# Kernel tuning notes

Hardware: AMD Instinct MI355X
Metric: run time of the kernel (lower is better)

Reference implementation:

```python
import jax, jax.numpy as jnp
import numpy as np

AVGF = 30   # number of averaged temporal segments (timesteps of the TTM)
TK = 10     # hardcoded number of transformer 'layers' in the source
HA = 1      # hardcoded number of heads


def _ln(v, g, b, eps=1e-5):
    # LayerNorm over the last (only) dim of a 1-D vector
    mu = jnp.mean(v)
    var = jnp.mean((v - mu) ** 2)
    return (v - mu) / jnp.sqrt(var + eps) * g + b


def setup_inputs() -> dict:
    key = jax.random.key(0)
    ks = jax.random.split(key, 8)
    C, S, T = 32, 32, 360
    M = C * S  # 1024 = M_size1
    sc = 0.02  # scale randn params for numerical sanity (source uses raw randn)
    x = jax.random.normal(ks[0], (C, S, T), jnp.float32)
    weight = jax.random.normal(ks[1], (M, M), jnp.float32) * sc
    Wq = jax.random.normal(ks[2], (TK, HA, M // HA, M), jnp.float32) * sc
    Wk = jax.random.normal(ks[3], (TK, HA, M // HA, M), jnp.float32) * sc
    Wv = jax.random.normal(ks[4], (TK, HA, M // HA, M), jnp.float32) * sc
    Wo = jax.random.normal(ks[5], (TK, M, M), jnp.float32) * sc
    ln_g = jnp.ones((M,), jnp.float32); ln_b = jnp.zeros((M,), jnp.float32)
    lnz_g = jnp.ones((M,), jnp.float32); lnz_b = jnp.zeros((M,), jnp.float32)
    fc1_w = jax.random.normal(ks[6], (4 * M, M), jnp.float32) * sc
    fc1_b = jnp.zeros((4 * M,), jnp.float32)
    fc2_w = jax.random.normal(ks[7], (M, 4 * M), jnp.float32) * sc
    fc2_b = jnp.zeros((M,), jnp.float32)
    return dict(x=x, weight=weight, Wq=Wq, Wk=Wk, Wv=Wv, Wo=Wo,
                ln_g=ln_g, ln_b=ln_b, lnz_g=lnz_g, lnz_b=lnz_b,
                fc1_w=fc1_w, fc1_b=fc1_b, fc2_w=fc2_w, fc2_b=fc2_b)


def reference(x, weight, Wq, Wk, Wv, Wo, ln_g, ln_b, lnz_g, lnz_b,
              fc1_w, fc1_b, fc2_w, fc2_b):
    C, S, T = x.shape
    M = C * S
    seg = T // AVGF
    Dh = M // HA
    # redefine(): transpose(0,2) then segment-average over the temporal dim, flatten
    xcf = jnp.transpose(x, (2, 1, 0)).reshape(AVGF, seg, S * C).mean(axis=1)  # (AVGF, M)
    # sinusoidal positional 'bias' exactly as the source loop builds it
    i = jnp.arange(AVGF, dtype=jnp.float32)[:, None]
    j = jnp.arange(0, M, 2, dtype=jnp.float32)[None, :]
    ang = i / jnp.power(jnp.float32(10000.0), 2.0 * j / M)
    pe = jnp.zeros((AVGF, M), jnp.float32).at[:, 0::2].set(jnp.sin(ang)).at[:, 1::2].set(jnp.cos(ang))
    s0 = xcf @ weight.T + pe  # savespace init: weight @ x[i] + bias
    scale = 1.0 / jnp.sqrt(jnp.float32(Dh))

    def step(vcum, s):
        # vcum[a]: sum over previously processed timesteps of r*v at layer a
        for a in range(TK):
            z = _ln(s, ln_g, ln_b)
            q = jnp.einsum('hdm,m->hd', Wq[a], z)  # (HA, Dh)
            k = jnp.einsum('hdm,m->hd', Wk[a], z)
            v = jnp.einsum('hdm,m->hd', Wv[a], z)
            score = jnp.sum(q * scale * k, axis=-1)          # (HA,) scalar per head
            r = jax.nn.softmax(score[:, None], axis=-1)[:, 0]  # softmax of a scalar == 1
            rv = r[:, None] * v
            s = Wo[a] @ vcum[a].reshape(-1) + s              # imv = sum over subj < i
            s = _ln(s, lnz_g, lnz_b) + s
            s = fc2_w @ jax.nn.gelu(fc1_w @ s + fc1_b, approximate=False) + fc2_b
            vcum = vcum.at[a].add(rv)                        # current timestep now visible to future
        return vcum, s

    vcum0 = jnp.zeros((TK, HA, Dh), jnp.float32)
    _, out = jax.lax.scan(step, vcum0, s0)  # sequential over timesteps
    return out.reshape(AVGF, S, C)
```

## Files before the change

### kernel.cpp

```cpp
#include <hip/hip_runtime.h>

#define MDIM 1024
#define H4   4096
#define TKL  10
#define NT   30
#define NWFR 39
#define GBLK 256
#define GTHR 1024
#define AGENT __HIP_MEMORY_SCOPE_AGENT

typedef _Float16 h2v __attribute__((ext_vector_type(2)));
typedef unsigned int uv4 __attribute__((ext_vector_type(4)));
typedef float fv4 __attribute__((ext_vector_type(4)));
union U16 { uv4 u; h2v h[4]; _Float16 f[8]; };

__device__ __forceinline__ float wred(float v) {
#pragma unroll
  for (int o = 32; o; o >>= 1) v += __shfl_xor(v, o, 64);
  return v;
}

__device__ __forceinline__ float dot16(const U16& w, const U16& x, float acc) {
  acc = __builtin_amdgcn_fdot2(w.h[0], x.h[0], acc, false);
  acc = __builtin_amdgcn_fdot2(w.h[1], x.h[1], acc, false);
  acc = __builtin_amdgcn_fdot2(w.h[2], x.h[2], acc, false);
  acc = __builtin_amdgcn_fdot2(w.h[3], x.h[3], acc, false);
  return acc;
}

__device__ __forceinline__ void stg16(const void* p, uv4 v) {
  asm volatile("global_store_dwordx4 %0, %1, off sc0 sc1" :: "v"(p), "v"(v) : "memory");
}

__global__ void k_cvt(const float* __restrict__ in, _Float16* __restrict__ out, int n8) {
  int g = blockIdx.x * blockDim.x + threadIdx.x;
  if (g >= n8) return;
  const float4* p = (const float4*)in;
  float4 a = p[2 * g], b = p[2 * g + 1];
  U16 o;
  o.f[0] = (_Float16)a.x; o.f[1] = (_Float16)a.y;
  o.f[2] = (_Float16)a.z; o.f[3] = (_Float16)a.w;
  o.f[4] = (_Float16)b.x; o.f[5] = (_Float16)b.y;
  o.f[6] = (_Float16)b.z; o.f[7] = (_Float16)b.w;
  ((uv4*)out)[g] = o.u;
}

__global__ void k_xcf(const float* __restrict__ x, float* __restrict__ xcf) {
  int idx = blockIdx.x * blockDim.x + threadIdx.x;
  if (idx >= NT * MDIM) return;
  int i = idx >> 10, m = idx & (MDIM - 1);
  int c = m & 31, s = m >> 5;
  const float* p = x + c * (32 * 360) + s * 360 + i * 12;
  float acc = 0.f;
#pragma unroll
  for (int k = 0; k < 12; ++k) acc += p[k];
  xcf[idx] = acc * (1.0f / 12.0f);
}

__global__ void k_s0(const float* __restrict__ xcf, const float* __restrict__ W,
                     float* __restrict__ S, float* __restrict__ Smir) {
  int wid = (blockIdx.x * blockDim.x + threadIdx.x) >> 6;
  int lane = threadIdx.x & 63;
  if (wid >= NT * MDIM) return;
  int i = wid >> 10, m = wid & (MDIM - 1);
  const float4* wr = (const float4*)(W + (size_t)m * MDIM);
  const float4* xr = (const float4*)(xcf + i * MDIM);
  float acc = 0.f;
#pragma unroll
  for (int k = 0; k < 4; ++k) {
    float4 w = wr[lane + (k << 6)];
    float4 xv = xr[lane + (k << 6)];
    acc += w.x * xv.x + w.y * xv.y + w.z * xv.z + w.w * xv.w;
  }
  acc = wred(acc);
  if (lane == 0) {
    int e = m & ~1;
    float ang = (float)i / powf(10000.0f, (float)e / 512.0f);
    float pe = (m & 1) ? cosf(ang) : sinf(ang);
    float val = acc + pe;
    S[wid] = val;
    Smir[((size_t)i * NT + i) * MDIM + m] = val;
  }
}

__device__ __forceinline__ void gbar(unsigned* bar, unsigned ep) {
  asm volatile("s_waitcnt vmcnt(0)" ::: "memory");
  __syncthreads();
  if (threadIdx.x == 0) {
    unsigned* leaf = bar + ((blockIdx.x & 7) << 5);
    const unsigned prev = __hip_atomic_fetch_add(leaf, 1u, __ATOMIC_RELAXED, AGENT);
    if (prev == ep * 32u - 1u) {
      const unsigned r = __hip_atomic_fetch_add(bar + 256, 1u, __ATOMIC_RELAXED, AGENT);
      if (r == ep * 8u - 1u)
        __hip_atomic_store(bar + 288, ep, __ATOMIC_RELAXED, AGENT);
    }
    while (__hip_atomic_load(bar + 288, __ATOMIC_RELAXED, AGENT) < ep)
      __builtin_amdgcn_s_sleep(2);
  }
  __syncthreads();
}

__global__ __launch_bounds__(GTHR) void k_main(
    const _Float16* __restrict__ Wvh, const _Float16* __restrict__ Woh,
    const _Float16* __restrict__ fc1h, const float* __restrict__ fc1b,
    const _Float16* __restrict__ fc2h, const float* __restrict__ fc2b,
    const float* __restrict__ lng, const float* __restrict__ lnb,
    const float* __restrict__ lzg, const float* __restrict__ lzb,
    float* __restrict__ S, float* __restrict__ ocum,
    float* __restrict__ Smir, float* __restrict__ Omir, float* __restrict__ vmir,
    _Float16* __restrict__ hmir, unsigned* __restrict__ bar) {
  __shared__ __align__(16) _Float16 WoL[32 * MDIM];
  __shared__ __align__(16) _Float16 fc1L[16 * MDIM];
  __shared__ __align__(16) _Float16 fc2L[4 * H4];
  __shared__ __align__(16) _Float16 zxL[10 * MDIM];
  __shared__ __align__(16) float4 stats[TKL];
  __shared__ __align__(16) float vOut[40];
  __shared__ __align__(16) _Float16 hgel[TKL][16];
  __shared__ float part[4][4][TKL];
  __shared__ __align__(16) float sOut[TKL][4];
  _Float16* zL = zxL;
  _Float16* x2L = zxL + 5 * MDIM;
  _Float16* vL = zxL;

  const int tid = threadIdx.x;
  const int lane = tid & 63;
  const int bwave = tid >> 6;
  const int b = blockIdx.x;
  unsigned ep = 0;

  __builtin_amdgcn_fence(__ATOMIC_ACQUIRE, "agent");

#pragma unroll
  for (int it = 0; it < 2; ++it) {
    const int idx = tid + (it << 10);
    ((uv4*)fc1L)[idx] = ((const uv4*)(fc1h + (size_t)b * 16384))[idx];
    ((uv4*)fc2L)[idx] = ((const uv4*)(fc2h + (size_t)b * 16384))[idx];
  }
#pragma unroll
  for (int it = 0; it < 4; ++it) {
    const int idx = tid + (it << 10);
    const int row = idx >> 7, off = idx & 127;
    const int layer = row >> 2, q = row & 3;
    ((uv4*)WoL)[idx] =
        *(const uv4*)(Woh + ((size_t)layer << 20) + ((size_t)((b << 2) + q) << 10) + (off << 3));
  }
  __syncthreads();

  for (int t = 0; t < NWFR; ++t) {
    const int alo = (t - (NT - 1)) > 0 ? (t - (NT - 1)) : 0;
    const int ahi = t < (TKL - 1) ? t : (TKL - 1);
    const int nc = ahi - alo + 1;
    const float* Smirt = Smir + (size_t)t * NT * MDIM;
    const float* Omirt = Omir + (size_t)t * TKL * MDIM;

    if (bwave < nc) {
      const int a = alo + bwave, i = t - a;
      const fv4* sp = (const fv4*)(Smirt + (size_t)i * MDIM + (lane << 4));
      const fv4* op = (const fv4*)(Omirt + (size_t)a * MDIM + (lane << 4));
      fv4 sv[4], tv[4];
#pragma unroll
      for (int k = 0; k < 4; ++k) { sv[k] = sp[k]; tv[k] = sv[k] + op[k]; }
      float s1 = 0.f, t1 = 0.f;
#pragma unroll
      for (int k = 0; k < 4; ++k)
#pragma unroll
        for (int e = 0; e < 4; ++e) { s1 += sv[k][e]; t1 += tv[k][e]; }
      const float mu_s = wred(s1) * (1.0f / MDIM);
      const float mu_t = wred(t1) * (1.0f / MDIM);
      float s2 = 0.f, t2 = 0.f;
#pragma unroll
      for (int k = 0; k < 4; ++k)
#pragma unroll
        for (int e = 0; e < 4; ++e) {
          float d = sv[k][e] - mu_s; s2 += d * d;
          float f = tv[k][e] - mu_t; t2 += f * f;
        }
      const float var_s = wred(s2) * (1.0f / MDIM);
      const float var_t = wred(t2) * (1.0f / MDIM);
      if (!lane)
        stats[bwave] = make_float4(mu_s, rsqrtf(var_s + 1e-5f),
                                   mu_t, rsqrtf(var_t + 1e-5f));
    }
    __syncthreads();

#pragma unroll
    for (int ch = 0; ch < 2; ++ch) {
      const int c0 = ch * 5;
      if (c0 < nc) {
        {
          const int cp = tid >> 7, e = (tid & 127) << 3;
          const int c = c0 + cp;
          if (cp < 5 && c < nc) {
            const int a = alo + c, i = t - a;
            const float4 st4 = stats[c];
            fv4 sA = *(const fv4*)(Smirt + (size_t)i * MDIM + e);
            fv4 sB = *(const fv4*)(Smirt + (size_t)i * MDIM + e + 4);
            fv4 oA = *(const fv4*)(Omirt + (size_t)a * MDIM + e);
            fv4 oB = *(const fv4*)(Omirt + (size_t)a * MDIM + e + 4);
            fv4 g1A = *(const fv4*)(lng + e), g1B = *(const fv4*)(lng + e + 4);
            fv4 b1A = *(const fv4*)(lnb + e), b1B = *(const fv4*)(lnb + e + 4);
            fv4 g2A = *(const fv4*)(lzg + e), g2B = *(const fv4*)(lzg + e + 4);
            fv4 b2A = *(const fv4*)(lzb + e), b2B = *(const fv4*)(lzb + e + 4);
            U16 zz, xx;
#pragma unroll
            for (int k = 0; k < 4; ++k) {
              zz.f[k] = (_Float16)((sA[k] - st4.x) * st4.y * g1A[k] + b1A[k]);
              zz.f[4 + k] = (_Float16)((sB[k] - st4.x) * st4.y * g1B[k] + b1B[k]);
              const float u0 = sA[k] + oA[k], u1 = sB[k] + oB[k];
              xx.f[k] = (_Float16)((u0 - st4.z) * st4.w * g2A[k] + b2A[k] + u0);
              xx.f[4 + k] = (_Float16)((u1 - st4.z) * st4.w * g2B[k] + b2B[k] + u1);
            }
            *(uv4*)(zL + cp * MDIM + e) = zz.u;
            *(uv4*)(x2L + cp * MDIM + e) = xx.u;
          }
        }
        __syncthreads();
        {
          const int rw = bwave;
          U16 f0, f1;
          f0.u = *(const uv4*)(fc1L + rw * MDIM + (lane << 3));
          f1.u = *(const uv4*)(fc1L + rw * MDIM + 512 + (lane << 3));
          float sel = 0.f;
#pragma unroll
          for (int cc = 0; cc < 5; ++cc) {
            const int c = c0 + cc;
            if (c < nc) {
              U16 x0, x1;
              x0.u = *(const uv4*)(x2L + cc * MDIM + (lane << 3));
              x1.u = *(const uv4*)(x2L + cc * MDIM + 512 + (lane << 3));
              float acc = dot16(f0, x0, 0.f);
              acc = dot16(f1, x1, acc);
              acc = wred(acc);
              sel = (lane == cc) ? acc : sel;
            }
          }
          const float xg = sel + fc1b[(b << 4) | rw];
          const float ge = 0.5f * xg * (1.0f + erff(xg * 0.70710678118654752f));
          if (lane < 5 && c0 + lane < nc) hgel[c0 + lane][rw] = (_Float16)ge;
        }
#pragma unroll
        for (int k = 0; k < 2; ++k) {
          const int j = bwave + (k << 4);
          if (j < 20) {
            const int rc = j >> 2, c = c0 + rc;
            if (c < nc) {
              const int layer = alo + c;
              if (t - layer != NT - 1) {
                const _Float16* wp = Wvh + ((size_t)layer << 20) +
                                     ((size_t)((b << 2) + (j & 3)) << 10);
                U16 w0, w1, z0, z1;
                w0.u = *(const uv4*)(wp + (lane << 3));
                w1.u = *(const uv4*)(wp + 512 + (lane << 3));
                z0.u = *(const uv4*)(zL + rc * MDIM + (lane << 3));
                z1.u = *(const uv4*)(zL + rc * MDIM + 512 + (lane << 3));
                float acc = dot16(w0, z0, 0.f);
                acc = dot16(w1, z1, acc);
                acc = wred(acc);
                if (!lane) vOut[(c << 2) + (j & 3)] = acc;
              }
            }
          }
        }
        __syncthreads();
      }
    }
    if (tid < TKL && tid < nc && (t - (alo + tid)) != NT - 1)
      stg16(vmir + ((size_t)t * TKL + alo + tid) * MDIM + (b << 2),
            __builtin_bit_cast(uv4, *(const fv4*)&vOut[tid << 2]));
    if (bwave < nc && lane < 2)
      stg16(hmir + ((size_t)t * TKL + alo + bwave) * H4 + (b << 4) + (lane << 3),
            *(const uv4*)&hgel[bwave][lane << 3]);
    ++ep; gbar(bar, ep);

#pragma unroll
    for (int c = 0; c < TKL; ++c)
      if (c < nc && (t - (alo + c)) != NT - 1)
        vL[c * MDIM + tid] = (_Float16)vmir[((size_t)t * TKL + alo + c) * MDIM + tid];
    __syncthreads();
#pragma unroll
    for (int k = 0; k < 3; ++k) {
      const int j = bwave + (k << 4);
      if (j < 40) {
        const int c = j >> 2;
        if (c < nc) {
          const int layer = alo + c;
          if (layer < 8 && t - layer != NT - 1) {
            const _Float16* wp = WoL + ((layer << 2) + (j & 3)) * MDIM;
            U16 w0, w1, v0, v1;
            w0.u = *(const uv4*)(wp + (lane << 3));
            w1.u = *(const uv4*)(wp + 512 + (lane << 3));
            v0.u = *(const uv4*)(vL + c * MDIM + (lane << 3));
            v1.u = *(const uv4*)(vL + c * MDIM + 512 + (lane << 3));
            float acc = dot16(w0, v0, 0.f);
            acc = dot16(w1, v1, acc);
            acc = wred(acc);
            if (!lane) vOut[j] = acc;
          }
        }
      }
    }
#pragma unroll
    for (int k = 0; k < 3; ++k) {
      const int j = bwave + (k << 4);
      if (j < 40) {
        const int c = j >> 2;
        if (c < nc) {
          const int layer = alo + c;
          if (layer >= 8 && t - layer != NT - 1) {
            const _Float16* wp = Woh + ((size_t)layer << 20) +
                                 ((size_t)((b << 2) + (j & 3)) << 10);
            U16 w0, w1, v0, v1;
            w0.u = *(const uv4*)(wp + (lane << 3));
            w1.u = *(const uv4*)(wp + 512 + (lane << 3));
            v0.u = *(const uv4*)(vL + c * MDIM + (lane << 3));
            v1.u = *(const uv4*)(vL + c * MDIM + 512 + (lane << 3));
            float acc = dot16(w0, v0, 0.f);
            acc = dot16(w1, v1, acc);
            acc = wred(acc);
            if (!lane) vOut[j] = acc;
          }
        }
      }
    }
    {
      const int rl = bwave >> 2, kq = bwave & 3;
      U16 w2a, w2b;
      w2a.u = *(const uv4*)(fc2L + rl * H4 + (kq << 10) + (lane << 3));
      w2b.u = *(const uv4*)(fc2L + rl * H4 + (kq << 10) + 512 + (lane << 3));
#pragma unroll
      for (int c = 0; c < TKL; ++c)
        if (c < nc) {
          U16 h0, h1;
          const _Float16* hp = hmir + ((size_t)t * TKL + alo + c) * H4 + (kq << 10);
          h0.u = *(const uv4*)(hp + (lane << 3));
          h1.u = *(const uv4*)(hp + 512 + (lane << 3));
          float acc = dot16(w2a, h0, 0.f);
          acc = dot16(w2b, h1, acc);
          acc = wred(acc);
          if (!lane) part[rl][kq][c] = acc;
        }
    }
    __syncthreads();
    if (tid < TKL && tid < nc && (t - (alo + tid)) != NT - 1) {
      const int layer = alo + tid;
      float* po = ocum + layer * MDIM + (b << 2);
      fv4 o = *(const fv4*)po;
      o += *(const fv4*)&vOut[tid << 2];
      *(fv4*)po = o;
      stg16(Omir + ((size_t)(t + 1) * TKL + layer) * MDIM + (b << 2),
            __builtin_bit_cast(uv4, o));
    }
    if (bwave < nc && lane < 4)
      sOut[bwave][lane] = part[lane][0][bwave] + part[lane][1][bwave] +
                          part[lane][2][bwave] + part[lane][3][bwave] +
                          fc2b[(b << 2) | lane];
    __syncthreads();
    if (bwave < nc && !lane) {
      const int a = alo + bwave, i = t - a;
      fv4 sv = *(const fv4*)(&sOut[bwave][0]);
      if (a == TKL - 1)
        *(fv4*)(S + (size_t)i * MDIM + (b << 2)) = sv;
      else
        stg16(Smir + ((size_t)(t + 1) * NT + i) * MDIM + (b << 2),
              __builtin_bit_cast(uv4, sv));
    }
    ++ep; gbar(bar, ep);
  }
}

extern "C" void kernel_launch(void* const* d_in, const int* in_sizes, int n_in,
                              void* d_out, int out_size, void* d_ws, size_t ws_size,
                              hipStream_t stream) {
  const float* x    = (const float*)d_in[0];
  const float* W    = (const float*)d_in[1];
  const float* Wv   = (const float*)d_in[4];
  const float* Wo   = (const float*)d_in[5];
  const float* lng  = (const float*)d_in[6];
  const float* lnb  = (const float*)d_in[7];
  const float* lzg  = (const float*)d_in[8];
  const float* lzb  = (const float*)d_in[9];
  const float* fc1w = (const float*)d_in[10];
  const float* fc1b = (const float*)d_in[11];
  const float* fc2w = (const float*)d_in[12];
  const float* fc2b = (const float*)d_in[13];
  float* S = (float*)d_out;

  float* xcf  = (float*)d_ws;
  float* ocum = xcf + 30720;
  unsigned* bar = (unsigned*)(ocum + 10240);
  float* Smir = (float*)(bar + 512);
  float* Omir = Smir + 1228800;
  float* vmir = Omir + 409600;
  _Float16* hmir = (_Float16*)(vmir + 409600);
  _Float16* Wvh  = hmir + 1638400;
  _Float16* Woh  = Wvh + 10485760;
  _Float16* fc1h = Woh + 10485760;
  _Float16* fc2h = fc1h + 4194304;

  hipLaunchKernelGGL(k_cvt, dim3(5120), dim3(256), 0, stream, Wv, Wvh, 1310720);
  hipLaunchKernelGGL(k_cvt, dim3(5120), dim3(256), 0, stream, Wo, Woh, 1310720);
  hipLaunchKernelGGL(k_cvt, dim3(2048), dim3(256), 0, stream, fc1w, fc1h, 524288);
  hipLaunchKernelGGL(k_cvt, dim3(2048), dim3(256), 0, stream, fc2w, fc2h, 524288);
  hipLaunchKernelGGL(k_xcf, dim3((NT * MDIM + 255) / 256), dim3(256), 0, stream, x, xcf);
  hipLaunchKernelGGL(k_s0, dim3(NT * MDIM / 4), dim3(256), 0, stream, xcf, W, S, Smir);
  hipMemsetAsync(ocum, 0, 10240 * sizeof(float), stream);
  hipMemsetAsync(Omir, 0, 409600 * sizeof(float), stream);
  hipMemsetAsync(bar, 0, 2048, stream);

  hipLaunchKernelGGL(k_main, dim3(GBLK), dim3(GTHR), 0, stream,
                     Wvh, Woh, fc1h, fc1b, fc2h, fc2b, lng, lnb, lzg, lzb,
                     S, ocum, Smir, Omir, vmir, hmir, bar);
}
```

Before: 862.1 us.

## Use MFMA on a dedicated wave for fc1/fc2 and overlap with Wv/Wo dots

The fc1 and fc2 matrix-vector products, previously spread across all 16 waves with fdot2 and cross-lane reductions, are moved onto wave 0 using 16x16x32 f16 MFMA instructions. The other 15 waves concurrently compute the Wv and Wo dot products. The two 5-column chunks are merged into a single pass with full 10-column LDS buffers, which removes a barrier and the partial-sum reduction stage. fc2 weights are now read from global memory instead of LDS, freeing shared memory. The risk is that one wave serially handles the whole K=4096 fc2 loop and becomes the critical path.

```diff
diff --git a/kernel.cpp b/kernel.cpp
--- a/kernel.cpp
+++ b/kernel.cpp
@@ -10,6 +10,8 @@
 #define AGENT __HIP_MEMORY_SCOPE_AGENT
 
 typedef _Float16 h2v __attribute__((ext_vector_type(2)));
+typedef _Float16 f16x8 __attribute__((ext_vector_type(8)));
+typedef float f32x4 __attribute__((ext_vector_type(4)));
 typedef unsigned int uv4 __attribute__((ext_vector_type(4)));
 typedef float fv4 __attribute__((ext_vector_type(4)));
 union U16 { uv4 u; h2v h[4]; _Float16 f[8]; };
@@ -100,7 +102,7 @@
   __syncthreads();
 }
 
-__global__ __launch_bounds__(GTHR) void k_main(
+__global__ __launch_bounds__(GTHR, 4) void k_main(
     const _Float16* __restrict__ Wvh, const _Float16* __restrict__ Woh,
     const _Float16* __restrict__ fc1h, const float* __restrict__ fc1b,
     const _Float16* __restrict__ fc2h, const float* __restrict__ fc2b,
@@ -111,16 +113,12 @@
     _Float16* __restrict__ hmir, unsigned* __restrict__ bar) {
   __shared__ __align__(16) _Float16 WoL[32 * MDIM];
   __shared__ __align__(16) _Float16 fc1L[16 * MDIM];
-  __shared__ __align__(16) _Float16 fc2L[4 * H4];
-  __shared__ __align__(16) _Float16 zxL[10 * MDIM];
+  __shared__ __align__(16) _Float16 zL[TKL * MDIM];
+  __shared__ __align__(16) _Float16 x2L[TKL * MDIM];
   __shared__ __align__(16) float4 stats[TKL];
   __shared__ __align__(16) float vOut[40];
   __shared__ __align__(16) _Float16 hgel[TKL][16];
-  __shared__ float part[4][4][TKL];
-  __shared__ __align__(16) float sOut[TKL][4];
-  _Float16* zL = zxL;
-  _Float16* x2L = zxL + 5 * MDIM;
-  _Float16* vL = zxL;
+  _Float16* vL = zL;
 
   const int tid = threadIdx.x;
   const int lane = tid & 63;
@@ -134,7 +132,6 @@
   for (int it = 0; it < 2; ++it) {
     const int idx = tid + (it << 10);
     ((uv4*)fc1L)[idx] = ((const uv4*)(fc1h + (size_t)b * 16384))[idx];
-    ((uv4*)fc2L)[idx] = ((const uv4*)(fc2h + (size_t)b * 16384))[idx];
   }
 #pragma unroll
   for (int it = 0; it < 4; ++it) {
@@ -184,86 +181,86 @@
     __syncthreads();
 
 #pragma unroll
-    for (int ch = 0; ch < 2; ++ch) {
-      const int c0 = ch * 5;
-      if (c0 < nc) {
-        {
-          const int cp = tid >> 7, e = (tid & 127) << 3;
-          const int c = c0 + cp;
-          if (cp < 5 && c < nc) {
-            const int a = alo + c, i = t - a;
-            const float4 st4 = stats[c];
-            fv4 sA = *(const fv4*)(Smirt + (size_t)i * MDIM + e);
-            fv4 sB = *(const fv4*)(Smirt + (size_t)i * MDIM + e + 4);
-            fv4 oA = *(const fv4*)(Omirt + (size_t)a * MDIM + e);
-            fv4 oB = *(const fv4*)(Omirt + (size_t)a * MDIM + e + 4);
-            fv4 g1A = *(const fv4*)(lng + e), g1B = *(const fv4*)(lng + e + 4);
-            fv4 b1A = *(const fv4*)(lnb + e), b1B = *(const fv4*)(lnb + e + 4);
-            fv4 g2A = *(const fv4*)(lzg + e), g2B = *(const fv4*)(lzg + e + 4);
-            fv4 b2A = *(const fv4*)(lzb + e), b2B = *(const fv4*)(lzb + e + 4);
-            U16 zz, xx;
-#pragma unroll
-            for (int k = 0; k < 4; ++k) {
-              zz.f[k] = (_Float16)((sA[k] - st4.x) * st4.y * g1A[k] + b1A[k]);
-              zz.f[4 + k] = (_Float16)((sB[k] - st4.x) * st4.y * g1B[k] + b1B[k]);
-              const float u0 = sA[k] + oA[k], u1 = sB[k] + oB[k];
-              xx.f[k] = (_Float16)((u0 - st4.z) * st4.w * g2A[k] + b2A[k] + u0);
-              xx.f[4 + k] = (_Float16)((u1 - st4.z) * st4.w * g2B[k] + b2B[k] + u1);
-            }
-            *(uv4*)(zL + cp * MDIM + e) = zz.u;
-            *(uv4*)(x2L + cp * MDIM + e) = xx.u;
-          }
-        }
-        __syncthreads();
-        {
-          const int rw = bwave;
-          U16 f0, f1;
-          f0.u = *(const uv4*)(fc1L + rw * MDIM + (lane << 3));
-          f1.u = *(const uv4*)(fc1L + rw * MDIM + 512 + (lane << 3));
-          float sel = 0.f;
-#pragma unroll
-          for (int cc = 0; cc < 5; ++cc) {
-            const int c = c0 + cc;
-            if (c < nc) {
-              U16 x0, x1;
-              x0.u = *(const uv4*)(x2L + cc * MDIM + (lane << 3));
-              x1.u = *(const uv4*)(x2L + cc * MDIM + 512 + (lane << 3));
-              float acc = dot16(f0, x0, 0.f);
-              acc = dot16(f1, x1, acc);
+    for (int p = 0; p < 2; ++p) {
+      const int cp = tid >> 7, c = p * 5 + cp;
+      if (cp < 5 && c < nc) {
+        const int a = alo + c, i = t - a;
+        const int e = (tid & 127) << 3;
+        const float4 st4 = stats[c];
+        fv4 sA = *(const fv4*)(Smirt + (size_t)i * MDIM + e);
+        fv4 sB = *(const fv4*)(Smirt + (size_t)i * MDIM + e + 4);
+        fv4 oA = *(const fv4*)(Omirt + (size_t)a * MDIM + e);
+        fv4 oB = *(const fv4*)(Omirt + (size_t)a * MDIM + e + 4);
+        fv4 g1A = *(const fv4*)(lng + e), g1B = *(const fv4*)(lng + e + 4);
+        fv4 b1A = *(const fv4*)(lnb + e), b1B = *(const fv4*)(lnb + e + 4);
+        fv4 g2A = *(const fv4*)(lzg + e), g2B = *(const fv4*)(lzg + e + 4);
+        fv4 b2A = *(const fv4*)(lzb + e), b2B = *(const fv4*)(lzb + e + 4);
+        U16 zz, xx;
+#pragma unroll
+        for (int k = 0; k < 4; ++k) {
+          zz.f[k] = (_Float16)((sA[k] - st4.x) * st4.y * g1A[k] + b1A[k]);
+          zz.f[4 + k] = (_Float16)((sB[k] - st4.x) * st4.y * g1B[k] + b1B[k]);
+          const float u0 = sA[k] + oA[k], u1 = sB[k] + oB[k];
+          xx.f[k] = (_Float16)((u0 - st4.z) * st4.w * g2A[k] + b2A[k] + u0);
+          xx.f[4 + k] = (_Float16)((u1 - st4.z) * st4.w * g2B[k] + b2B[k] + u1);
+        }
+        *(uv4*)(zL + c * MDIM + e) = zz.u;
+        *(uv4*)(x2L + c * MDIM + e) = xx.u;
+      }
+    }
+    __syncthreads();
+
+    if (bwave == 0) {
+      const int r16 = lane & 15;
+      const int kg = (lane >> 4) << 3;
+      const int bc = r16 < TKL ? r16 : TKL - 1;
+      f32x4 d0 = {0.f, 0.f, 0.f, 0.f}, d1 = {0.f, 0.f, 0.f, 0.f};
+#pragma unroll
+      for (int k0 = 0; k0 < MDIM; k0 += 64) {
+        f16x8 a0 = *(const f16x8*)(fc1L + r16 * MDIM + k0 + kg);
+        f16x8 b0 = *(const f16x8*)(x2L + bc * MDIM + k0 + kg);
+        d0 = __builtin_amdgcn_mfma_f32_16x16x32_f16(a0, b0, d0, 0, 0, 0);
+        f16x8 a1 = *(const f16x8*)(fc1L + r16 * MDIM + k0 + 32 + kg);
+        f16x8 b1 = *(const f16x8*)(x2L + bc * MDIM + k0 + 32 + kg);
+        d1 = __builtin_amdgcn_mfma_f32_16x16x32_f16(a1, b1, d1, 0, 0, 0);
+      }
+      const int dcol = lane & 15;
+      const int drow0 = (lane >> 4) << 2;
+      if (dcol < nc) {
+        fv4 bias = *(const fv4*)(fc1b + (b << 4) + drow0);
+#pragma unroll
+        for (int r = 0; r < 4; ++r) {
+          const float xg = d0[r] + d1[r] + bias[r];
+          hgel[dcol][drow0 + r] =
+              (_Float16)(0.5f * xg * (1.0f + erff(xg * 0.70710678118654752f)));
+        }
+      }
+    } else {
+#pragma unroll
+      for (int k = 0; k < 3; ++k) {
+        const int j = (bwave - 1) + 15 * k;
+        if (j < 40) {
+          const int c = j >> 2;
+          if (c < nc) {
+            const int layer = alo + c;
+            if (t - layer != NT - 1) {
+              const _Float16* wp = Wvh + ((size_t)layer << 20) +
+                                   ((size_t)((b << 2) + (j & 3)) << 10);
+              U16 w0, w1, z0, z1;
+              w0.u = *(const uv4*)(wp + (lane << 3));
+              w1.u = *(const uv4*)(wp + 512 + (lane << 3));
+              z0.u = *(const uv4*)(zL + c * MDIM + (lane << 3));
+              z1.u = *(const uv4*)(zL + c * MDIM + 512 + (lane << 3));
+              float acc = dot16(w0, z0, 0.f);
+              acc = dot16(w1, z1, acc);
               acc = wred(acc);
-              sel = (lane == cc) ? acc : sel;
+              if (!lane) vOut[j] = acc;
             }
           }
-          const float xg = sel + fc1b[(b << 4) | rw];
-          const float ge = 0.5f * xg * (1.0f + erff(xg * 0.70710678118654752f));
-          if (lane < 5 && c0 + lane < nc) hgel[c0 + lane][rw] = (_Float16)ge;
-        }
-#pragma unroll
-        for (int k = 0; k < 2; ++k) {
-          const int j = bwave + (k << 4);
-          if (j < 20) {
-            const int rc = j >> 2, c = c0 + rc;
-            if (c < nc) {
-              const int layer = alo + c;
-              if (t - layer != NT - 1) {
-                const _Float16* wp = Wvh + ((size_t)layer << 20) +
-                                     ((size_t)((b << 2) + (j & 3)) << 10);
-                U16 w0, w1, z0, z1;
-                w0.u = *(const uv4*)(wp + (lane << 3));
-                w1.u = *(const uv4*)(wp + 512 + (lane << 3));
-                z0.u = *(const uv4*)(zL + rc * MDIM + (lane << 3));
-                z1.u = *(const uv4*)(zL + rc * MDIM + 512 + (lane << 3));
-                float acc = dot16(w0, z0, 0.f);
-                acc = dot16(w1, z1, acc);
-                acc = wred(acc);
-                if (!lane) vOut[(c << 2) + (j & 3)] = acc;
-              }
-            }
-          }
-        }
-        __syncthreads();
-      }
-    }
+        }
+      }
+    }
+    __syncthreads();
     if (tid < TKL && tid < nc && (t - (alo + tid)) != NT - 1)
       stg16(vmir + ((size_t)t * TKL + alo + tid) * MDIM + (b << 2),
             __builtin_bit_cast(uv4, *(const fv4*)&vOut[tid << 2]));
@@ -277,68 +274,81 @@
       if (c < nc && (t - (alo + c)) != NT - 1)
         vL[c * MDIM + tid] = (_Float16)vmir[((size_t)t * TKL + alo + c) * MDIM + tid];
     __syncthreads();
-#pragma unroll
-    for (int k = 0; k < 3; ++k) {
-      const int j = bwave + (k << 4);
-      if (j < 40) {
-        const int c = j >> 2;
-        if (c < nc) {
-          const int layer = alo + c;
-          if (layer < 8 && t - layer != NT - 1) {
-            const _Float16* wp = WoL + ((layer << 2) + (j & 3)) * MDIM;
-            U16 w0, w1, v0, v1;
-            w0.u = *(const uv4*)(wp + (lane << 3));
-            w1.u = *(const uv4*)(wp + 512 + (lane << 3));
-            v0.u = *(const uv4*)(vL + c * MDIM + (lane << 3));
-            v1.u = *(const uv4*)(vL + c * MDIM + 512 + (lane << 3));
-            float acc = dot16(w0, v0, 0.f);
-            acc = dot16(w1, v1, acc);
-            acc = wred(acc);
-            if (!lane) vOut[j] = acc;
+    if (bwave == 0) {
+      const int r4 = lane & 3;
+      const int kg = (lane >> 4) << 3;
+      const int colc = lane & 15;
+      const int aCl = (alo + colc) < ahi ? (alo + colc) : ahi;
+      const _Float16* Ap = fc2h + ((size_t)((b << 2) | r4) << 12);
+      const _Float16* Bp = hmir + ((size_t)t * TKL + aCl) * H4;
+      f32x4 d0 = {0.f, 0.f, 0.f, 0.f}, d1 = {0.f, 0.f, 0.f, 0.f};
+#pragma unroll 8
+      for (int k0 = 0; k0 < H4; k0 += 64) {
+        f16x8 a0 = *(const f16x8*)(Ap + k0 + kg);
+        f16x8 b0 = *(const f16x8*)(Bp + k0 + kg);
+        d0 = __builtin_amdgcn_mfma_f32_16x16x32_f16(a0, b0, d0, 0, 0, 0);
+        f16x8 a1 = *(const f16x8*)(Ap + k0 + 32 + kg);
+        f16x8 b1 = *(const f16x8*)(Bp + k0 + 32 + kg);
+        d1 = __builtin_amdgcn_mfma_f32_16x16x32_f16(a1, b1, d1, 0, 0, 0);
+      }
+      if (lane < 16 && lane < nc) {
+        const int a = alo + lane, i = t - a;
+        fv4 bias = *(const fv4*)(fc2b + (b << 2));
+        fv4 sv;
+#pragma unroll
+        for (int r = 0; r < 4; ++r) sv[r] = d0[r] + d1[r] + bias[r];
+        if (a == TKL - 1)
+          *(fv4*)(S + (size_t)i * MDIM + (b << 2)) = sv;
+        else
+          stg16(Smir + ((size_t)(t + 1) * NT + i) * MDIM + (b << 2),
+                __builtin_bit_cast(uv4, sv));
+      }
+    } else {
+#pragma unroll
+      for (int k = 0; k < 3; ++k) {
+        const int j = (bwave - 1) + 15 * k;
+        if (j < 40) {
+          const int c = j >> 2;
+          if (c < nc) {
+            const int layer = alo + c;
+            if (layer < 8 && t - layer != NT - 1) {
+              const _Float16* wp = WoL + ((layer << 2) + (j & 3)) * MDIM;
+              U16 w0, w1, v0, v1;
+              w0.u = *(const uv4*)(wp + (lane << 3));
+              w1.u = *(const uv4*)(wp + 512 + (lane << 3));
+              v0.u = *(const uv4*)(vL + c * MDIM + (lane << 3));
+              v1.u = *(const uv4*)(vL + c * MDIM + 512 + (lane << 3));
+              float acc = dot16(w0, v0, 0.f);
+              acc = dot16(w1, v1, acc);
+              acc = wred(acc);
+              if (!lane) vOut[j] = acc;
+            }
           }
         }
       }
-    }
-#pragma unroll
-    for (int k = 0; k < 3; ++k) {
-      const int j = bwave + (k << 4);
-      if (j < 40) {
-        const int c = j >> 2;
-        if (c < nc) {
-          const int layer = alo + c;
-          if (layer >= 8 && t - layer != NT - 1) {
-            const _Float16* wp = Woh + ((size_t)layer << 20) +
-                                 ((size_t)((b << 2) + (j & 3)) << 10);
-            U16 w0, w1, v0, v1;
-            w0.u = *(const uv4*)(wp + (lane << 3));
-            w1.u = *(const uv4*)(wp + 512 + (lane << 3));
-            v0.u = *(const uv4*)(vL + c * MDIM + (lane << 3));
-            v1.u = *(const uv4*)(vL + c * MDIM + 512 + (lane << 3));
-            float acc = dot16(w0, v0, 0.f);
-            acc = dot16(w1, v1, acc);
-            acc = wred(acc);
-            if (!lane) vOut[j] = acc;
+#pragma unroll
+      for (int k = 0; k < 3; ++k) {
+        const int j = (bwave - 1) + 15 * k;
+        if (j < 40) {
+          const int c = j >> 2;
+          if (c < nc) {
+            const int layer = alo + c;
+            if (layer >= 8 && t - layer != NT - 1) {
+              const _Float16* wp = Woh + ((size_t)layer << 20) +
+                                   ((size_t)((b << 2) + (j & 3)) << 10);
+              U16 w0, w1, v0, v1;
+              w0.u = *(const uv4*)(wp + (lane << 3));
+              w1.u = *(const uv4*)(wp + 512 + (lane << 3));
+              v0.u = *(const uv4*)(vL + c * MDIM + (lane << 3));
+              v1.u = *(const uv4*)(vL + c * MDIM + 512 + (lane << 3));
+              float acc = dot16(w0, v0, 0.f);
+              acc = dot16(w1, v1, acc);
+              acc = wred(acc);
+              if (!lane) vOut[j] = acc;
+            }
           }
         }
       }
-    }
-    {
-      const int rl = bwave >> 2, kq = bwave & 3;
-      U16 w2a, w2b;
-      w2a.u = *(const uv4*)(fc2L + rl * H4 + (kq << 10) + (lane << 3));
-      w2b.u = *(const uv4*)(fc2L + rl * H4 + (kq << 10) + 512 + (lane << 3));
-#pragma unroll
-      for (int c = 0; c < TKL; ++c)
-        if (c < nc) {
-          U16 h0, h1;
-          const _Float16* hp = hmir + ((size_t)t * TKL + alo + c) * H4 + (kq << 10);
-          h0.u = *(const uv4*)(hp + (lane << 3));
-          h1.u = *(const uv4*)(hp + 512 + (lane << 3));
-          float acc = dot16(w2a, h0, 0.f);
-          acc = dot16(w2b, h1, acc);
-          acc = wred(acc);
-          if (!lane) part[rl][kq][c] = acc;
-        }
     }
     __syncthreads();
     if (tid < TKL && tid < nc && (t - (alo + tid)) != NT - 1) {
@@ -349,20 +359,6 @@
       *(fv4*)po = o;
       stg16(Omir + ((size_t)(t + 1) * TKL + layer) * MDIM + (b << 2),
             __builtin_bit_cast(uv4, o));
-    }
-    if (bwave < nc && lane < 4)
-      sOut[bwave][lane] = part[lane][0][bwave] + part[lane][1][bwave] +
-                          part[lane][2][bwave] + part[lane][3][bwave] +
-                          fc2b[(b << 2) | lane];
-    __syncthreads();
-    if (bwave < nc && !lane) {
-      const int a = alo + bwave, i = t - a;
-      fv4 sv = *(const fv4*)(&sOut[bwave][0]);
-      if (a == TKL - 1)
-        *(fv4*)(S + (size_t)i * MDIM + (b << 2)) = sv;
-      else
-        stg16(Smir + ((size_t)(t + 1) * NT + i) * MDIM + (b << 2),
-              __builtin_bit_cast(uv4, sv));
     }
     ++ep; gbar(bar, ep);
   }
```

New measurement: 1.643 ms. 90.6% more time.
